# Optimization experiments

Hardware: AMD Instinct MI355X
Metric: run time of the kernel (lower is better)

## Reference

```python
import jax, jax.numpy as jnp
import numpy as np

EPS = 1e-5
TAU = 0.1

def _bn(x, g, b):
    # BatchNorm1d in training mode: batch statistics (biased variance)
    mu = jnp.mean(x, axis=0, keepdims=True)
    var = jnp.var(x, axis=0, keepdims=True)
    return (x - mu) * jax.lax.rsqrt(var + EPS) * g + b

def setup_inputs():
    key = jax.random.key(0)
    ks = jax.random.split(key, 8)
    B, D, H, L, P, C, ND, NP = 32768, 2048, 1024, 384, 192, 10, 2, 2
    s = 0.02
    u = jax.random.uniform(ks[7], (B, NP), minval=1e-6, maxval=1.0 - 1e-6)
    return {
        'x': jax.random.normal(ks[0], (B, D), dtype=jnp.float32),
        'W_pre': jax.random.normal(ks[1], (H, D), dtype=jnp.float32) * s,
        'b_pre': jnp.zeros((H,), jnp.float32),
        'g_pre': jnp.ones((H,), jnp.float32),
        'be_pre': jnp.zeros((H,), jnp.float32),
        'W_disc': jax.random.normal(ks[2], (L, H), dtype=jnp.float32) * s,
        'b_disc': jnp.zeros((L,), jnp.float32),
        'g_disc': jnp.ones((L,), jnp.float32),
        'be_disc': jnp.zeros((L,), jnp.float32),
        'W_dfc': jax.random.normal(ks[3], (ND, L), dtype=jnp.float32) * s,
        'b_dfc': jnp.zeros((ND,), jnp.float32),
        'W_sw': jax.random.normal(ks[4], (NP, L), dtype=jnp.float32) * s,
        'b_sw': jnp.zeros((NP,), jnp.float32),
        'W1': jax.random.normal(ks[5], (NP, P, H), dtype=jnp.float32) * s,
        'b1': jnp.zeros((NP, P), jnp.float32),
        'W2': jax.random.normal(ks[6], (NP, C, P), dtype=jnp.float32) * s,
        'b2': jnp.zeros((NP, C), jnp.float32),
        'gumbel_noise': -jnp.log(-jnp.log(u)),
    }

def reference(x, W_pre, b_pre, g_pre, be_pre, W_disc, b_disc, g_disc, be_disc,
              W_dfc, b_dfc, W_sw, b_sw, W1, b1, W2, b2, gumbel_noise):
    # pre_classifier: Linear + BN + ReLU
    feature = jax.nn.relu(_bn(x @ W_pre.T + b_pre, g_pre, be_pre))
    # GRL is identity in forward
    dp = jax.nn.relu(_bn(feature @ W_disc.T + b_disc, g_disc, be_disc))
    dom = dp @ W_dfc.T + b_dfc                      # [B, num_domains]
    sw = jax.nn.relu(dp @ W_sw.T + b_sw)            # [B, n_partition]
    gum = jax.nn.softmax((sw + gumbel_noise) / TAU, axis=-1)  # soft gumbel-softmax
    idx = jnp.argmax(gum, axis=-1)                  # [B] routing decision
    # compute both (tiny) experts densely, then select per sample (faithful math,
    # avoids per-sample gather of full weight matrices)
    h_all = jax.nn.relu(jnp.einsum('bd,epd->bep', feature, W1) + b1)  # [B,E,P]
    o_all = jnp.einsum('bep,ecp->bec', h_all, W2) + b2                # [B,E,C]
    out = jnp.take_along_axis(o_all, idx[:, None, None], axis=1)[:, 0]  # [B,C]
    # original: sum_p gum[b,p] * stacked (stacked has one entry) == out * sum(gum)
    cop = out * jnp.sum(gum, axis=-1, keepdims=True)
    return cop, dom, idx
```

## Files before the change

kernel.cpp:

```cpp
#include <hip/hip_runtime.h>
#include <math.h>

#define kB 32768
#define kD 2048
#define kH 1024
#define kL 384
#define kP 192
#define kC 10
#define kNP 2
#define kND 2
#define kNCAT 768
#define kTAU 0.1f
#define kEPS 1e-5f
#define NPART 256
#define SCALE 64.0f
#define INV_SC2 (1.0f / 4096.0f)

typedef _Float16 f16x8 __attribute__((ext_vector_type(8)));
typedef _Float16 f16x4 __attribute__((ext_vector_type(4)));
typedef float f32x4 __attribute__((ext_vector_type(4)));

__device__ __forceinline__ void gll16(const unsigned short* g, unsigned short* l)
{
    __builtin_amdgcn_global_load_lds(
        (const __attribute__((address_space(1))) unsigned int*)g,
        (__attribute__((address_space(3))) unsigned int*)l, 16, 0, 0);
}

__global__ __launch_bounds__(256)
void split_pack(const float* __restrict__ in, unsigned short* __restrict__ out, int K)
{
    const int row = blockIdx.x;
    const int t = threadIdx.x;
    const int s = row & 7;
    const float* ir = in + (size_t)row * K;
    unsigned short* orow = out + (size_t)row * (K * 2);
    for (int k0 = t * 4; k0 < K; k0 += 1024) {
        const float4 v = *(const float4*)&ir[k0];
        const float a0 = v.x * SCALE, a1 = v.y * SCALE, a2 = v.z * SCALE, a3 = v.w * SCALE;
        const _Float16 h0 = (_Float16)a0, h1 = (_Float16)a1, h2 = (_Float16)a2, h3 = (_Float16)a3;
        const _Float16 l0 = (_Float16)(a0 - (float)h0), l1 = (_Float16)(a1 - (float)h1);
        const _Float16 l2 = (_Float16)(a2 - (float)h2), l3 = (_Float16)(a3 - (float)h3);
        const f16x4 hi = {h0, h1, h2, h3};
        const f16x4 lo = {l0, l1, l2, l3};
        const int kb = k0 >> 5, kk = k0 & 31;
        const int c = kk >> 3, off = kk & 7;
        *(f16x4*)&orow[kb * 64 + ((c ^ s) << 3) + off]       = hi;
        *(f16x4*)&orow[kb * 64 + (((c ^ 4) ^ s) << 3) + off] = lo;
    }
}

template<int KDIM, bool BN>
__global__ __launch_bounds__(512, 1)
void gemm_fused(const float* __restrict__ Afp,
                const unsigned short* __restrict__ Bpk,
                const float* __restrict__ bnsc, const float* __restrict__ bnsh,
                float* __restrict__ C, const int N, const int gridX,
                float* __restrict__ psum, float* __restrict__ psumsq, const int statN)
{
    constexpr int NKB = KDIM / 32;
    __shared__ unsigned short lds[4][256 * 64];

    const int t = threadIdx.x;
    const int lane = t & 63;
    const int w = t >> 6;
    const int wr = w >> 2, wc = w & 3;
    const int lr = lane & 15, lg = lane >> 4;
    const int ca = (lg ^ (lr & 7)) * 8;

    const int nwg = gridDim.x;
    const int chunk = nwg >> 3;
    const int bid = blockIdx.x;
    const int logical = (bid & 7) * chunk + (bid >> 3);
    const int bx = logical % gridX, by = logical / gridX;
    const int m0 = by * 256, n0 = bx * 256;

    const int arow = t >> 1;
    const int akh = t & 1;
    const int s7 = arow & 7;
    const int c0 = akh * 2, c1 = akh * 2 + 1;
    const float* aSrc = Afp + (size_t)(m0 + arow) * KDIM + akh * 16;

    const size_t bstride = (size_t)NKB * 64;
    const unsigned short* bG[4];
    int bLoff[4];
#pragma unroll
    for (int it = 0; it < 4; ++it) {
        const int Q = (w * 4 + it) * 64 + lane;
        bG[it] = Bpk + (size_t)(n0 + (Q >> 3)) * bstride + (Q & 7) * 8;
        bLoff[it] = (w * 4 + it) * 512;
    }

    f32x4 acc[8][4];
#pragma unroll
    for (int mi = 0; mi < 8; ++mi)
#pragma unroll
        for (int ni = 0; ni < 4; ++ni) acc[mi][ni] = (f32x4){0.f, 0.f, 0.f, 0.f};

    float4 av[4], scv[4], shv[4];

    auto stage_issue = [&](int kb, int buf) {
        const int kt = kb * 32;
#pragma unroll
        for (int it = 0; it < 4; ++it)
            gll16(bG[it] + (size_t)kb * 64, &lds[2 + buf][bLoff[it]]);
#pragma unroll
        for (int j = 0; j < 4; ++j)
            av[j] = *(const float4*)&aSrc[kt + j * 4];
        if constexpr (BN) {
#pragma unroll
            for (int j = 0; j < 4; ++j) {
                scv[j] = *(const float4*)&bnsc[kt + akh * 16 + j * 4];
                shv[j] = *(const float4*)&bnsh[kt + akh * 16 + j * 4];
            }
        }
    };

    auto stage_write = [&](int buf) {
        float v[16];
#pragma unroll
        for (int j = 0; j < 4; ++j) {
            float4 a = av[j];
            if constexpr (BN) {
                a.x = fmaxf(fmaf(a.x, scv[j].x, shv[j].x), 0.f);
                a.y = fmaxf(fmaf(a.y, scv[j].y, shv[j].y), 0.f);
                a.z = fmaxf(fmaf(a.z, scv[j].z, shv[j].z), 0.f);
                a.w = fmaxf(fmaf(a.w, scv[j].w, shv[j].w), 0.f);
            } else {
                a.x *= SCALE; a.y *= SCALE; a.z *= SCALE; a.w *= SCALE;
            }
            v[j * 4 + 0] = a.x; v[j * 4 + 1] = a.y;
            v[j * 4 + 2] = a.z; v[j * 4 + 3] = a.w;
        }
        f16x8 hi[2], lo[2];
#pragma unroll
        for (int h = 0; h < 2; ++h)
#pragma unroll
            for (int i = 0; i < 8; ++i) {
                const float x = v[h * 8 + i];
                const _Float16 hh = (_Float16)x;
                hi[h][i] = hh;
                lo[h][i] = (_Float16)(x - (float)hh);
            }
        unsigned short* dst = &lds[buf][arow * 64];
        *(f16x8*)&dst[(c0 ^ s7) * 8]       = hi[0];
        *(f16x8*)&dst[(c1 ^ s7) * 8]       = hi[1];
        *(f16x8*)&dst[((c0 ^ 4) ^ s7) * 8] = lo[0];
        *(f16x8*)&dst[((c1 ^ 4) ^ s7) * 8] = lo[1];
    };

    stage_issue(0, 0);
    stage_write(0);
    asm volatile("s_waitcnt vmcnt(0) lgkmcnt(0)" ::: "memory");
    __builtin_amdgcn_s_barrier();

    for (int kb = 0; kb < NKB; ++kb) {
        const int cur = kb & 1, nxt = cur ^ 1;
        const bool pf = (kb + 1 < NKB);
        if (pf) stage_issue(kb + 1, nxt);

        f16x8 bh[4], bl[4];
#pragma unroll
        for (int ni = 0; ni < 4; ++ni) {
            const unsigned short* bb = &lds[2 + cur][(wc * 64 + ni * 16 + lr) * 64];
            bh[ni] = *(const f16x8*)&bb[ca];
            bl[ni] = *(const f16x8*)&bb[ca ^ 32];
        }
#pragma unroll
        for (int mi = 0; mi < 8; ++mi) {
            const unsigned short* ab = &lds[cur][(wr * 128 + mi * 16 + lr) * 64];
            const f16x8 ah = *(const f16x8*)&ab[ca];
            const f16x8 al = *(const f16x8*)&ab[ca ^ 32];
#pragma unroll
            for (int ni = 0; ni < 4; ++ni)
                acc[mi][ni] = __builtin_amdgcn_mfma_f32_16x16x32_f16(ah, bh[ni], acc[mi][ni], 0, 0, 0);
#pragma unroll
            for (int ni = 0; ni < 4; ++ni)
                acc[mi][ni] = __builtin_amdgcn_mfma_f32_16x16x32_f16(ah, bl[ni], acc[mi][ni], 0, 0, 0);
#pragma unroll
            for (int ni = 0; ni < 4; ++ni)
                acc[mi][ni] = __builtin_amdgcn_mfma_f32_16x16x32_f16(al, bh[ni], acc[mi][ni], 0, 0, 0);
        }
        if (pf) stage_write(nxt);
        asm volatile("s_waitcnt vmcnt(0) lgkmcnt(0)" ::: "memory");
        __builtin_amdgcn_s_barrier();
    }

#pragma unroll
    for (int mi = 0; mi < 8; ++mi)
#pragma unroll
        for (int j = 0; j < 4; ++j) {
            const int row = m0 + wr * 128 + mi * 16 + lg * 4 + j;
            float* cr = C + (size_t)row * N + n0 + wc * 64 + lr;
#pragma unroll
            for (int ni = 0; ni < 4; ++ni) cr[ni * 16] = acc[mi][ni][j];
        }

#pragma unroll
    for (int ni = 0; ni < 4; ++ni) {
        float s = 0.f, sq = 0.f;
#pragma unroll
        for (int mi = 0; mi < 8; ++mi)
#pragma unroll
            for (int j = 0; j < 4; ++j) {
                const float v = acc[mi][ni][j];
                s += v;
                sq = fmaf(v, v, sq);
            }
        s  += __shfl_xor(s, 16);  s  += __shfl_xor(s, 32);
        sq += __shfl_xor(sq, 16); sq += __shfl_xor(sq, 32);
        const int col = n0 + wc * 64 + ni * 16 + lr;
        if (lane < 16 && col < statN) {
            psum[(size_t)(by * 2 + wr) * statN + col]   = s;
            psumsq[(size_t)(by * 2 + wr) * statN + col] = sq;
        }
    }
}

__global__ __launch_bounds__(256)
void colstat_finalize(const float* __restrict__ psum, const float* __restrict__ psumsq,
                      int ncols, const float* __restrict__ g, const float* __restrict__ be,
                      float* __restrict__ scale, float* __restrict__ shift,
                      float inv_sc, float outsc)
{
    const int c = blockIdx.x * 256 + threadIdx.x;
    if (c >= ncols) return;
    float s = 0.f, sq = 0.f;
    for (int i = 0; i < NPART; ++i) {
        s  += psum[(size_t)i * ncols + c];
        sq += psumsq[(size_t)i * ncols + c];
    }
    const float mup = s * (1.f / kB);
    const float var = (sq * (1.f / kB) - mup * mup) * inv_sc * inv_sc;
    const float scl = outsc * g[c] * rsqrtf(var + kEPS) * inv_sc;
    scale[c] = scl;
    shift[c] = fmaf(-mup, scl, outsc * be[c]);
}

__global__ __launch_bounds__(256)
void tail_kernel(const float* __restrict__ Z2,
                 const float* __restrict__ scale2, const float* __restrict__ shift2,
                 const float* __restrict__ W_dfc, const float* __restrict__ b_dfc,
                 const float* __restrict__ W_sw, const float* __restrict__ b_sw,
                 const float* __restrict__ b1, const float* __restrict__ W2,
                 const float* __restrict__ b2, const float* __restrict__ noise,
                 float* __restrict__ out)
{
    __shared__ float sWdfc[kND * kL];
    __shared__ float sWsw[kNP * kL];
    __shared__ float sW2[kNP * kC * kP];
    __shared__ float sb1[kNP * kP];
    __shared__ float sScale[kL];
    __shared__ float sShift[kL];
    const int t = threadIdx.x;
    for (int i = t; i < kND * kL; i += 256) sWdfc[i] = W_dfc[i];
    for (int i = t; i < kNP * kL; i += 256) sWsw[i] = W_sw[i];
    for (int i = t; i < kNP * kC * kP; i += 256) sW2[i] = W2[i];
    for (int i = t; i < kNP * kP; i += 256) sb1[i] = b1[i];
    for (int i = t; i < kL; i += 256) { sScale[i] = scale2[i]; sShift[i] = shift2[i]; }
    __syncthreads();

    const int lane = t & 63;
    const int b = blockIdx.x * 4 + (t >> 6);
    const float* z = Z2 + (size_t)b * kNCAT;

    float d0 = 0.f, d1 = 0.f, s0 = 0.f, s1 = 0.f;
#pragma unroll
    for (int j = 0; j < 6; ++j) {
        const int k = lane + j * 64;
        const float dp = fmaxf(fmaf(z[k], sScale[k], sShift[k]), 0.f);
        d0 = fmaf(dp, sWdfc[k],      d0);
        d1 = fmaf(dp, sWdfc[kL + k], d1);
        s0 = fmaf(dp, sWsw[k],       s0);
        s1 = fmaf(dp, sWsw[kL + k],  s1);
    }
#pragma unroll
    for (int off = 32; off; off >>= 1) {
        d0 += __shfl_xor(d0, off);
        d1 += __shfl_xor(d1, off);
        s0 += __shfl_xor(s0, off);
        s1 += __shfl_xor(s1, off);
    }
    d0 += b_dfc[0];
    d1 += b_dfc[1];

    const float sw0 = fmaxf(s0 + b_sw[0], 0.f);
    const float sw1 = fmaxf(s1 + b_sw[1], 0.f);
    const float l0 = (sw0 + noise[(size_t)b * 2 + 0]) * (1.f / kTAU);
    const float l1 = (sw1 + noise[(size_t)b * 2 + 1]) * (1.f / kTAU);
    const float mx = fmaxf(l0, l1);
    const float e0 = expf(l0 - mx), e1 = expf(l1 - mx);
    const float inv = 1.f / (e0 + e1);
    const float sgum = e0 * inv + e1 * inv;
    const int idx = (l1 > l0) ? 1 : 0;

    const float* zh = z + kL + idx * kP;
    const float h0 = fmaxf(fmaf(zh[lane],       INV_SC2, sb1[idx * kP + lane]),       0.f);
    const float h1 = fmaxf(fmaf(zh[lane + 64],  INV_SC2, sb1[idx * kP + lane + 64]),  0.f);
    const float h2 = fmaxf(fmaf(zh[lane + 128], INV_SC2, sb1[idx * kP + lane + 128]), 0.f);

    float* cop  = out;
    float* dom  = out + (size_t)kB * kC;
    float* idxo = dom + (size_t)kB * kND;

#pragma unroll
    for (int c = 0; c < kC; ++c) {
        const float* wv = &sW2[(idx * kC + c) * kP];
        float oc = h0 * wv[lane] + h1 * wv[lane + 64] + h2 * wv[lane + 128];
#pragma unroll
        for (int off = 32; off; off >>= 1) oc += __shfl_xor(oc, off);
        if (lane == c) cop[(size_t)b * kC + c] = (oc + b2[idx * kC + c]) * sgum;
    }
    if (lane == 0) {
        dom[(size_t)b * 2 + 0] = d0;
        dom[(size_t)b * 2 + 1] = d1;
        idxo[b] = (float)idx;
    }
}

extern "C" void kernel_launch(void* const* d_in, const int* in_sizes, int n_in,
                              void* d_out, int out_size, void* d_ws, size_t ws_size,
                              hipStream_t stream)
{
    const float* x       = (const float*)d_in[0];
    const float* W_pre   = (const float*)d_in[1];
    const float* g_pre   = (const float*)d_in[3];
    const float* be_pre  = (const float*)d_in[4];
    const float* W_disc  = (const float*)d_in[5];
    const float* g_disc  = (const float*)d_in[7];
    const float* be_disc = (const float*)d_in[8];
    const float* W_dfc   = (const float*)d_in[9];
    const float* b_dfc   = (const float*)d_in[10];
    const float* W_sw    = (const float*)d_in[11];
    const float* b_sw    = (const float*)d_in[12];
    const float* W1      = (const float*)d_in[13];
    const float* b1      = (const float*)d_in[14];
    const float* W2      = (const float*)d_in[15];
    const float* b2      = (const float*)d_in[16];
    const float* noise   = (const float*)d_in[17];

    char* wsb = (char*)d_ws;
    unsigned short* Wps = (unsigned short*)wsb;
    unsigned short* Ws2 = (unsigned short*)(wsb + (size_t)1024 * 4096 * 2);
    float* Z1 = (float*)(wsb + (size_t)1024 * 4096 * 2 + (size_t)768 * 2048 * 2);
    float* Z2 = Z1 + (size_t)kB * kH;
    float* psum1  = Z2 + (size_t)kB * kNCAT;
    float* psq1   = psum1 + (size_t)NPART * kH;
    float* psum2  = psq1 + (size_t)NPART * kH;
    float* psq2   = psum2 + (size_t)NPART * kL;
    float* scale1 = psq2 + (size_t)NPART * kL;
    float* shift1 = scale1 + kH;
    float* scale2 = shift1 + kH;
    float* shift2 = scale2 + kL;
    float* out    = (float*)d_out;

    split_pack<<<dim3(kH), 256, 0, stream>>>(W_pre, Wps, kD);
    split_pack<<<dim3(kL), 256, 0, stream>>>(W_disc, Ws2, kH);
    split_pack<<<dim3(kNP * kP), 256, 0, stream>>>(W1, Ws2 + (size_t)kL * (2 * kH), kH);
    gemm_fused<kD, false><<<dim3(4 * 128), 512, 0, stream>>>(
        x, Wps, nullptr, nullptr, Z1, kH, 4, psum1, psq1, kH);
    colstat_finalize<<<dim3(kH / 256), 256, 0, stream>>>(psum1, psq1, kH, g_pre, be_pre,
                                                         scale1, shift1, INV_SC2, SCALE);
    gemm_fused<kH, true><<<dim3(3 * 128), 512, 0, stream>>>(
        Z1, Ws2, scale1, shift1, Z2, kNCAT, 3, psum2, psq2, kL);
    colstat_finalize<<<dim3((kL + 255) / 256), 256, 0, stream>>>(psum2, psq2, kL, g_disc, be_disc,
                                                                 scale2, shift2, INV_SC2, 1.0f);
    tail_kernel<<<dim3(kB / 4), 256, 0, stream>>>(Z2, scale2, shift2, W_dfc, b_dfc,
                                                  W_sw, b_sw, b1, W2, b2, noise, out);
}
```

Before: 650.5 us.

## Switch GEMM inner loop to 32x32x16 MFMA with new LDS swizzle key

```diff
diff --git a/kernel.cpp b/kernel.cpp
--- a/kernel.cpp
+++ b/kernel.cpp
@@ -18,7 +18,7 @@
 
 typedef _Float16 f16x8 __attribute__((ext_vector_type(8)));
 typedef _Float16 f16x4 __attribute__((ext_vector_type(4)));
-typedef float f32x4 __attribute__((ext_vector_type(4)));
+typedef float f32x16 __attribute__((ext_vector_type(16)));
 
 __device__ __forceinline__ void gll16(const unsigned short* g, unsigned short* l)
 {
@@ -27,12 +27,14 @@
         (__attribute__((address_space(3))) unsigned int*)l, 16, 0, 0);
 }
 
+__device__ __host__ __forceinline__ int key8(int r) { return (r ^ (r >> 3)) & 7; }
+
 __global__ __launch_bounds__(256)
 void split_pack(const float* __restrict__ in, unsigned short* __restrict__ out, int K)
 {
     const int row = blockIdx.x;
     const int t = threadIdx.x;
-    const int s = row & 7;
+    const int s = key8(row);
     const float* ir = in + (size_t)row * K;
     unsigned short* orow = out + (size_t)row * (K * 2);
     for (int k0 = t * 4; k0 < K; k0 += 1024) {
@@ -65,8 +67,7 @@
     const int lane = t & 63;
     const int w = t >> 6;
     const int wr = w >> 2, wc = w & 3;
-    const int lr = lane & 15, lg = lane >> 4;
-    const int ca = (lg ^ (lr & 7)) * 8;
+    const int l31 = lane & 31, kg = lane >> 5;
 
     const int nwg = gridDim.x;
     const int chunk = nwg >> 3;
@@ -77,7 +78,7 @@
 
     const int arow = t >> 1;
     const int akh = t & 1;
-    const int s7 = arow & 7;
+    const int skey = key8(arow);
     const int c0 = akh * 2, c1 = akh * 2 + 1;
     const float* aSrc = Afp + (size_t)(m0 + arow) * KDIM + akh * 16;
 
@@ -91,11 +92,21 @@
         bLoff[it] = (w * 4 + it) * 512;
     }
 
-    f32x4 acc[8][4];
-#pragma unroll
-    for (int mi = 0; mi < 8; ++mi)
-#pragma unroll
-        for (int ni = 0; ni < 4; ++ni) acc[mi][ni] = (f32x4){0.f, 0.f, 0.f, 0.f};
+    int keyA[4], keyB[2];
+#pragma unroll
+    for (int mi = 0; mi < 4; ++mi)
+        keyA[mi] = (l31 & 7) ^ ((mi * 4 + (l31 >> 3)) & 7);
+#pragma unroll
+    for (int ni = 0; ni < 2; ++ni)
+        keyB[ni] = (l31 & 7) ^ ((wc * 8 + ni * 4 + (l31 >> 3)) & 7);
+
+    f32x16 acc[4][2];
+#pragma unroll
+    for (int mi = 0; mi < 4; ++mi)
+#pragma unroll
+        for (int ni = 0; ni < 2; ++ni)
+#pragma unroll
+            for (int r = 0; r < 16; ++r) acc[mi][ni][r] = 0.f;
 
     float4 av[4], scv[4], shv[4];
 
@@ -143,10 +154,10 @@
                 lo[h][i] = (_Float16)(x - (float)hh);
             }
         unsigned short* dst = &lds[buf][arow * 64];
-        *(f16x8*)&dst[(c0 ^ s7) * 8]       = hi[0];
-        *(f16x8*)&dst[(c1 ^ s7) * 8]       = hi[1];
-        *(f16x8*)&dst[((c0 ^ 4) ^ s7) * 8] = lo[0];
-        *(f16x8*)&dst[((c1 ^ 4) ^ s7) * 8] = lo[1];
+        *(f16x8*)&dst[(c0 ^ skey) * 8]       = hi[0];
+        *(f16x8*)&dst[(c1 ^ skey) * 8]       = hi[1];
+        *(f16x8*)&dst[((c0 ^ 4) ^ skey) * 8] = lo[0];
+        *(f16x8*)&dst[((c1 ^ 4) ^ skey) * 8] = lo[1];
     };
 
     stage_issue(0, 0);
@@ -159,27 +170,35 @@
         const bool pf = (kb + 1 < NKB);
         if (pf) stage_issue(kb + 1, nxt);
 
-        f16x8 bh[4], bl[4];
-#pragma unroll
-        for (int ni = 0; ni < 4; ++ni) {
-            const unsigned short* bb = &lds[2 + cur][(wc * 64 + ni * 16 + lr) * 64];
-            bh[ni] = *(const f16x8*)&bb[ca];
-            bl[ni] = *(const f16x8*)&bb[ca ^ 32];
-        }
-#pragma unroll
-        for (int mi = 0; mi < 8; ++mi) {
-            const unsigned short* ab = &lds[cur][(wr * 128 + mi * 16 + lr) * 64];
-            const f16x8 ah = *(const f16x8*)&ab[ca];
-            const f16x8 al = *(const f16x8*)&ab[ca ^ 32];
-#pragma unroll
-            for (int ni = 0; ni < 4; ++ni)
-                acc[mi][ni] = __builtin_amdgcn_mfma_f32_16x16x32_f16(ah, bh[ni], acc[mi][ni], 0, 0, 0);
-#pragma unroll
-            for (int ni = 0; ni < 4; ++ni)
-                acc[mi][ni] = __builtin_amdgcn_mfma_f32_16x16x32_f16(ah, bl[ni], acc[mi][ni], 0, 0, 0);
-#pragma unroll
-            for (int ni = 0; ni < 4; ++ni)
-                acc[mi][ni] = __builtin_amdgcn_mfma_f32_16x16x32_f16(al, bh[ni], acc[mi][ni], 0, 0, 0);
+        f16x8 bh[2][2], bl[2][2];
+#pragma unroll
+        for (int ni = 0; ni < 2; ++ni) {
+            const unsigned short* bb = &lds[2 + cur][(wc * 64 + ni * 32 + l31) * 64];
+#pragma unroll
+            for (int ks = 0; ks < 2; ++ks) {
+                const int lg = ks * 2 + kg;
+                bh[ni][ks] = *(const f16x8*)&bb[((lg ^ keyB[ni]) << 3)];
+                bl[ni][ks] = *(const f16x8*)&bb[(((lg ^ 4) ^ keyB[ni]) << 3)];
+            }
+        }
+#pragma unroll
+        for (int mi = 0; mi < 4; ++mi) {
+            const unsigned short* ab = &lds[cur][(wr * 128 + mi * 32 + l31) * 64];
+            f16x8 ah[2], al[2];
+#pragma unroll
+            for (int ks = 0; ks < 2; ++ks) {
+                const int lg = ks * 2 + kg;
+                ah[ks] = *(const f16x8*)&ab[((lg ^ keyA[mi]) << 3)];
+                al[ks] = *(const f16x8*)&ab[(((lg ^ 4) ^ keyA[mi]) << 3)];
+            }
+#pragma unroll
+            for (int ni = 0; ni < 2; ++ni)
+#pragma unroll
+                for (int ks = 0; ks < 2; ++ks) {
+                    acc[mi][ni] = __builtin_amdgcn_mfma_f32_32x32x16_f16(ah[ks], bh[ni][ks], acc[mi][ni], 0, 0, 0);
+                    acc[mi][ni] = __builtin_amdgcn_mfma_f32_32x32x16_f16(ah[ks], bl[ni][ks], acc[mi][ni], 0, 0, 0);
+                    acc[mi][ni] = __builtin_amdgcn_mfma_f32_32x32x16_f16(al[ks], bh[ni][ks], acc[mi][ni], 0, 0, 0);
+                }
         }
         if (pf) stage_write(nxt);
         asm volatile("s_waitcnt vmcnt(0) lgkmcnt(0)" ::: "memory");
@@ -187,30 +206,32 @@
     }
 
 #pragma unroll
-    for (int mi = 0; mi < 8; ++mi)
-#pragma unroll
-        for (int j = 0; j < 4; ++j) {
-            const int row = m0 + wr * 128 + mi * 16 + lg * 4 + j;
-            float* cr = C + (size_t)row * N + n0 + wc * 64 + lr;
-#pragma unroll
-            for (int ni = 0; ni < 4; ++ni) cr[ni * 16] = acc[mi][ni][j];
-        }
-
-#pragma unroll
-    for (int ni = 0; ni < 4; ++ni) {
+    for (int mi = 0; mi < 4; ++mi)
+#pragma unroll
+        for (int ni = 0; ni < 2; ++ni) {
+            const int colg = n0 + wc * 64 + ni * 32 + l31;
+#pragma unroll
+            for (int r = 0; r < 16; ++r) {
+                const int row = m0 + wr * 128 + mi * 32 + (r & 3) + 8 * (r >> 2) + 4 * kg;
+                C[(size_t)row * N + colg] = acc[mi][ni][r];
+            }
+        }
+
+#pragma unroll
+    for (int ni = 0; ni < 2; ++ni) {
         float s = 0.f, sq = 0.f;
 #pragma unroll
-        for (int mi = 0; mi < 8; ++mi)
-#pragma unroll
-            for (int j = 0; j < 4; ++j) {
-                const float v = acc[mi][ni][j];
+        for (int mi = 0; mi < 4; ++mi)
+#pragma unroll
+            for (int r = 0; r < 16; ++r) {
+                const float v = acc[mi][ni][r];
                 s += v;
                 sq = fmaf(v, v, sq);
             }
-        s  += __shfl_xor(s, 16);  s  += __shfl_xor(s, 32);
-        sq += __shfl_xor(sq, 16); sq += __shfl_xor(sq, 32);
-        const int col = n0 + wc * 64 + ni * 16 + lr;
-        if (lane < 16 && col < statN) {
+        s  += __shfl_xor(s, 32);
+        sq += __shfl_xor(sq, 32);
+        const int col = n0 + wc * 64 + ni * 32 + l31;
+        if (lane < 32 && col < statN) {
             psum[(size_t)(by * 2 + wr) * statN + col]   = s;
             psumsq[(size_t)(by * 2 + wr) * statN + col] = sq;
         }
```

After: 691.1 us. +6.2%, slower.

## Deepen GEMM pipeline with two-stage A prefetch, LDS BN params, new swizzle, narrower tile

Applied to the files above, without the earlier changes.

```diff
diff --git a/kernel.cpp b/kernel.cpp
--- a/kernel.cpp
+++ b/kernel.cpp
@@ -20,6 +20,10 @@
 typedef _Float16 f16x4 __attribute__((ext_vector_type(4)));
 typedef float f32x4 __attribute__((ext_vector_type(4)));
 
+#define WAITVM4   asm volatile("s_waitcnt vmcnt(4)" ::: "memory")
+#define WAITVM0   asm volatile("s_waitcnt vmcnt(0)" ::: "memory")
+#define WAITLGKM0 asm volatile("s_waitcnt lgkmcnt(0)" ::: "memory")
+
 __device__ __forceinline__ void gll16(const unsigned short* g, unsigned short* l)
 {
     __builtin_amdgcn_global_load_lds(
@@ -27,12 +31,17 @@
         (__attribute__((address_space(3))) unsigned int*)l, 16, 0, 0);
 }
 
+__device__ __host__ __forceinline__ int wkey(int r)
+{
+    return (r & 1) | ((r & 2) << 1) | ((r & 4) >> 1);
+}
+
 __global__ __launch_bounds__(256)
 void split_pack(const float* __restrict__ in, unsigned short* __restrict__ out, int K)
 {
     const int row = blockIdx.x;
     const int t = threadIdx.x;
-    const int s = row & 7;
+    const int s = wkey(row & 7);
     const float* ir = in + (size_t)row * K;
     unsigned short* orow = out + (size_t)row * (K * 2);
     for (int k0 = t * 4; k0 < K; k0 += 1024) {
@@ -50,7 +59,7 @@
     }
 }
 
-template<int KDIM, bool BN>
+template<int KDIM, int TILEN, bool BN>
 __global__ __launch_bounds__(512, 1)
 void gemm_fused(const float* __restrict__ Afp,
                 const unsigned short* __restrict__ Bpk,
@@ -59,73 +68,77 @@
                 float* __restrict__ psum, float* __restrict__ psumsq, const int statN)
 {
     constexpr int NKB = KDIM / 32;
-    __shared__ unsigned short lds[4][256 * 64];
+    constexpr int NI = TILEN / 64;
+    constexpr int BG = TILEN / 64;
+    __shared__ __align__(16) unsigned short As_[2][256 * 64];
+    __shared__ __align__(16) unsigned short Bs_[2][TILEN * 64];
+    __shared__ float sScL[BN ? KDIM : 1];
+    __shared__ float sShL[BN ? KDIM : 1];
 
     const int t = threadIdx.x;
     const int lane = t & 63;
     const int w = t >> 6;
     const int wr = w >> 2, wc = w & 3;
     const int lr = lane & 15, lg = lane >> 4;
-    const int ca = (lg ^ (lr & 7)) * 8;
+    const int ca = (lg ^ wkey(lane & 7)) * 8;
 
     const int nwg = gridDim.x;
     const int chunk = nwg >> 3;
     const int bid = blockIdx.x;
     const int logical = (bid & 7) * chunk + (bid >> 3);
     const int bx = logical % gridX, by = logical / gridX;
-    const int m0 = by * 256, n0 = bx * 256;
+    const int m0 = by * 256, n0 = bx * TILEN;
 
     const int arow = t >> 1;
     const int akh = t & 1;
-    const int s7 = arow & 7;
+    const int skey = wkey(arow & 7);
     const int c0 = akh * 2, c1 = akh * 2 + 1;
     const float* aSrc = Afp + (size_t)(m0 + arow) * KDIM + akh * 16;
 
     const size_t bstride = (size_t)NKB * 64;
-    const unsigned short* bG[4];
-    int bLoff[4];
-#pragma unroll
-    for (int it = 0; it < 4; ++it) {
-        const int Q = (w * 4 + it) * 64 + lane;
+    const unsigned short* bG[BG];
+    int bLoff[BG];
+#pragma unroll
+    for (int it = 0; it < BG; ++it) {
+        const int Q = (w * BG + it) * 64 + lane;
         bG[it] = Bpk + (size_t)(n0 + (Q >> 3)) * bstride + (Q & 7) * 8;
-        bLoff[it] = (w * 4 + it) * 512;
-    }
-
-    f32x4 acc[8][4];
+        bLoff[it] = (w * BG + it) * 512;
+    }
+
+    f32x4 acc[8][NI];
 #pragma unroll
     for (int mi = 0; mi < 8; ++mi)
 #pragma unroll
-        for (int ni = 0; ni < 4; ++ni) acc[mi][ni] = (f32x4){0.f, 0.f, 0.f, 0.f};
-
-    float4 av[4], scv[4], shv[4];
-
-    auto stage_issue = [&](int kb, int buf) {
+        for (int ni = 0; ni < NI; ++ni) acc[mi][ni] = (f32x4){0.f, 0.f, 0.f, 0.f};
+
+    float4 av0[4], av1[4];
+
+    auto issueA = [&](float4 (&av)[4], int kb) {
         const int kt = kb * 32;
-#pragma unroll
-        for (int it = 0; it < 4; ++it)
-            gll16(bG[it] + (size_t)kb * 64, &lds[2 + buf][bLoff[it]]);
 #pragma unroll
         for (int j = 0; j < 4; ++j)
             av[j] = *(const float4*)&aSrc[kt + j * 4];
-        if constexpr (BN) {
-#pragma unroll
-            for (int j = 0; j < 4; ++j) {
-                scv[j] = *(const float4*)&bnsc[kt + akh * 16 + j * 4];
-                shv[j] = *(const float4*)&bnsh[kt + akh * 16 + j * 4];
-            }
-        }
     };
 
-    auto stage_write = [&](int buf) {
+    auto gllB = [&](int kb, int buf) {
+#pragma unroll
+        for (int it = 0; it < BG; ++it)
+            gll16(bG[it] + (size_t)kb * 64, &Bs_[buf][bLoff[it]]);
+    };
+
+    auto writeA = [&](const float4 (&av)[4], int buf, int tile) {
+        const int kt = tile * 32 + akh * 16;
         float v[16];
 #pragma unroll
         for (int j = 0; j < 4; ++j) {
             float4 a = av[j];
             if constexpr (BN) {
-                a.x = fmaxf(fmaf(a.x, scv[j].x, shv[j].x), 0.f);
-                a.y = fmaxf(fmaf(a.y, scv[j].y, shv[j].y), 0.f);
-                a.z = fmaxf(fmaf(a.z, scv[j].z, shv[j].z), 0.f);
-                a.w = fmaxf(fmaf(a.w, scv[j].w, shv[j].w), 0.f);
+                const float4 sc = *(const float4*)&sScL[kt + j * 4];
+                const float4 sh = *(const float4*)&sShL[kt + j * 4];
+                a.x = fmaxf(fmaf(a.x, sc.x, sh.x), 0.f);
+                a.y = fmaxf(fmaf(a.y, sc.y, sh.y), 0.f);
+                a.z = fmaxf(fmaf(a.z, sc.z, sh.z), 0.f);
+                a.w = fmaxf(fmaf(a.w, sc.w, sh.w), 0.f);
             } else {
                 a.x *= SCALE; a.y *= SCALE; a.z *= SCALE; a.w *= SCALE;
             }
@@ -142,48 +155,74 @@
                 hi[h][i] = hh;
                 lo[h][i] = (_Float16)(x - (float)hh);
             }
-        unsigned short* dst = &lds[buf][arow * 64];
-        *(f16x8*)&dst[(c0 ^ s7) * 8]       = hi[0];
-        *(f16x8*)&dst[(c1 ^ s7) * 8]       = hi[1];
-        *(f16x8*)&dst[((c0 ^ 4) ^ s7) * 8] = lo[0];
-        *(f16x8*)&dst[((c1 ^ 4) ^ s7) * 8] = lo[1];
+        unsigned short* dst = &As_[buf][arow * 64];
+        *(f16x8*)&dst[(c0 ^ skey) * 8]       = hi[0];
+        *(f16x8*)&dst[(c1 ^ skey) * 8]       = hi[1];
+        *(f16x8*)&dst[((c0 ^ 4) ^ skey) * 8] = lo[0];
+        *(f16x8*)&dst[((c1 ^ 4) ^ skey) * 8] = lo[1];
     };
 
-    stage_issue(0, 0);
-    stage_write(0);
-    asm volatile("s_waitcnt vmcnt(0) lgkmcnt(0)" ::: "memory");
-    __builtin_amdgcn_s_barrier();
-
-    for (int kb = 0; kb < NKB; ++kb) {
+    auto body = [&](int kb, const float4 (&avW)[4], float4 (&avI)[4]) {
         const int cur = kb & 1, nxt = cur ^ 1;
-        const bool pf = (kb + 1 < NKB);
-        if (pf) stage_issue(kb + 1, nxt);
-
-        f16x8 bh[4], bl[4];
-#pragma unroll
-        for (int ni = 0; ni < 4; ++ni) {
-            const unsigned short* bb = &lds[2 + cur][(wc * 64 + ni * 16 + lr) * 64];
+        if (kb + 1 < NKB) {
+            writeA(avW, nxt, kb + 1);
+            gllB(kb + 1, nxt);
+        }
+        __builtin_amdgcn_sched_barrier(0);
+        if (kb + 2 < NKB) issueA(avI, kb + 2);
+
+        f16x8 bh[NI], bl[NI];
+#pragma unroll
+        for (int ni = 0; ni < NI; ++ni) {
+            const unsigned short* bb = &Bs_[cur][(wc * (16 * NI) + ni * 16 + lr) * 64];
             bh[ni] = *(const f16x8*)&bb[ca];
             bl[ni] = *(const f16x8*)&bb[ca ^ 32];
         }
 #pragma unroll
         for (int mi = 0; mi < 8; ++mi) {
-            const unsigned short* ab = &lds[cur][(wr * 128 + mi * 16 + lr) * 64];
+            const unsigned short* ab = &As_[cur][(wr * 128 + mi * 16 + lr) * 64];
             const f16x8 ah = *(const f16x8*)&ab[ca];
             const f16x8 al = *(const f16x8*)&ab[ca ^ 32];
 #pragma unroll
-            for (int ni = 0; ni < 4; ++ni)
+            for (int ni = 0; ni < NI; ++ni)
                 acc[mi][ni] = __builtin_amdgcn_mfma_f32_16x16x32_f16(ah, bh[ni], acc[mi][ni], 0, 0, 0);
 #pragma unroll
-            for (int ni = 0; ni < 4; ++ni)
+            for (int ni = 0; ni < NI; ++ni)
                 acc[mi][ni] = __builtin_amdgcn_mfma_f32_16x16x32_f16(ah, bl[ni], acc[mi][ni], 0, 0, 0);
 #pragma unroll
-            for (int ni = 0; ni < 4; ++ni)
+            for (int ni = 0; ni < NI; ++ni)
                 acc[mi][ni] = __builtin_amdgcn_mfma_f32_16x16x32_f16(al, bh[ni], acc[mi][ni], 0, 0, 0);
         }
-        if (pf) stage_write(nxt);
-        asm volatile("s_waitcnt vmcnt(0) lgkmcnt(0)" ::: "memory");
-        __builtin_amdgcn_s_barrier();
+        if (kb + 1 < NKB) {
+            if (kb + 2 < NKB) { WAITVM4; } else { WAITVM0; }
+            WAITLGKM0;
+            __builtin_amdgcn_sched_barrier(0);
+            __builtin_amdgcn_s_barrier();
+            __builtin_amdgcn_sched_barrier(0);
+        }
+    };
+
+    if constexpr (BN) {
+        if (t < KDIM / 4) {
+            ((float4*)sScL)[t] = ((const float4*)bnsc)[t];
+            ((float4*)sShL)[t] = ((const float4*)bnsh)[t];
+        }
+        __syncthreads();
+    }
+    issueA(av0, 0);
+    gllB(0, 0);
+    __builtin_amdgcn_sched_barrier(0);
+    issueA(av1, 1);
+    writeA(av0, 0, 0);
+    WAITVM4;
+    WAITLGKM0;
+    __builtin_amdgcn_sched_barrier(0);
+    __builtin_amdgcn_s_barrier();
+    __builtin_amdgcn_sched_barrier(0);
+
+    for (int kb = 0; kb < NKB; kb += 2) {
+        body(kb,     av1, av0);
+        body(kb + 1, av0, av1);
     }
 
 #pragma unroll
@@ -191,13 +230,13 @@
 #pragma unroll
         for (int j = 0; j < 4; ++j) {
             const int row = m0 + wr * 128 + mi * 16 + lg * 4 + j;
-            float* cr = C + (size_t)row * N + n0 + wc * 64 + lr;
-#pragma unroll
-            for (int ni = 0; ni < 4; ++ni) cr[ni * 16] = acc[mi][ni][j];
-        }
-
-#pragma unroll
-    for (int ni = 0; ni < 4; ++ni) {
+            float* cr = C + (size_t)row * N + n0 + wc * (16 * NI) + lr;
+#pragma unroll
+            for (int ni = 0; ni < NI; ++ni) cr[ni * 16] = acc[mi][ni][j];
+        }
+
+#pragma unroll
+    for (int ni = 0; ni < NI; ++ni) {
         float s = 0.f, sq = 0.f;
 #pragma unroll
         for (int mi = 0; mi < 8; ++mi)
@@ -209,7 +248,7 @@
             }
         s  += __shfl_xor(s, 16);  s  += __shfl_xor(s, 32);
         sq += __shfl_xor(sq, 16); sq += __shfl_xor(sq, 32);
-        const int col = n0 + wc * 64 + ni * 16 + lr;
+        const int col = n0 + wc * (16 * NI) + ni * 16 + lr;
         if (lane < 16 && col < statN) {
             psum[(size_t)(by * 2 + wr) * statN + col]   = s;
             psumsq[(size_t)(by * 2 + wr) * statN + col] = sq;
@@ -357,12 +396,12 @@
     split_pack<<<dim3(kH), 256, 0, stream>>>(W_pre, Wps, kD);
     split_pack<<<dim3(kL), 256, 0, stream>>>(W_disc, Ws2, kH);
     split_pack<<<dim3(kNP * kP), 256, 0, stream>>>(W1, Ws2 + (size_t)kL * (2 * kH), kH);
-    gemm_fused<kD, false><<<dim3(4 * 128), 512, 0, stream>>>(
+    gemm_fused<kD, 256, false><<<dim3(4 * 128), 512, 0, stream>>>(
         x, Wps, nullptr, nullptr, Z1, kH, 4, psum1, psq1, kH);
     colstat_finalize<<<dim3(kH / 256), 256, 0, stream>>>(psum1, psq1, kH, g_pre, be_pre,
                                                          scale1, shift1, INV_SC2, SCALE);
-    gemm_fused<kH, true><<<dim3(3 * 128), 512, 0, stream>>>(
-        Z1, Ws2, scale1, shift1, Z2, kNCAT, 3, psum2, psq2, kL);
+    gemm_fused<kH, 128, true><<<dim3(6 * 128), 512, 0, stream>>>(
+        Z1, Ws2, scale1, shift1, Z2, kNCAT, 6, psum2, psq2, kL);
     colstat_finalize<<<dim3((kL + 255) / 256), 256, 0, stream>>>(psum2, psq2, kL, g_disc, be_disc,
                                                                  scale2, shift2, INV_SC2, 1.0f);
     tail_kernel<<<dim3(kB / 4), 256, 0, stream>>>(Z2, scale2, shift2, W_dfc, b_dfc,
```

Result: slower. 671.7 us (+3.3%).

## Shrink GEMM tiles to 128x128 with 256 threads, multiple blocks per CU

Applied to the files above, without the earlier changes.

```diff
diff --git a/kernel.cpp b/kernel.cpp
--- a/kernel.cpp
+++ b/kernel.cpp
@@ -12,7 +12,7 @@
 #define kNCAT 768
 #define kTAU 0.1f
 #define kEPS 1e-5f
-#define NPART 256
+#define NPART 512
 #define SCALE 64.0f
 #define INV_SC2 (1.0f / 4096.0f)
 
@@ -20,6 +20,12 @@
 typedef _Float16 f16x4 __attribute__((ext_vector_type(4)));
 typedef float f32x4 __attribute__((ext_vector_type(4)));
 
+#define WAITVM0   asm volatile("s_waitcnt vmcnt(0)" ::: "memory")
+#define WAITVM4   asm volatile("s_waitcnt vmcnt(4)" ::: "memory")
+#define WAITLGKM0 asm volatile("s_waitcnt lgkmcnt(0)" ::: "memory")
+#define SB0       __builtin_amdgcn_sched_barrier(0)
+#define BAR       __builtin_amdgcn_s_barrier()
+
 __device__ __forceinline__ void gll16(const unsigned short* g, unsigned short* l)
 {
     __builtin_amdgcn_global_load_lds(
@@ -27,12 +33,17 @@
         (__attribute__((address_space(3))) unsigned int*)l, 16, 0, 0);
 }
 
+__device__ __host__ __forceinline__ int wkey(int r)
+{
+    return (r & 1) | ((r & 2) << 1) | ((r & 4) >> 1);
+}
+
 __global__ __launch_bounds__(256)
 void split_pack(const float* __restrict__ in, unsigned short* __restrict__ out, int K)
 {
     const int row = blockIdx.x;
     const int t = threadIdx.x;
-    const int s = row & 7;
+    const int s = wkey(row & 7);
     const float* ir = in + (size_t)row * K;
     unsigned short* orow = out + (size_t)row * (K * 2);
     for (int k0 = t * 4; k0 < K; k0 += 1024) {
@@ -51,7 +62,7 @@
 }
 
 template<int KDIM, bool BN>
-__global__ __launch_bounds__(512, 1)
+__global__ __launch_bounds__(256, 3)
 void gemm_fused(const float* __restrict__ Afp,
                 const unsigned short* __restrict__ Bpk,
                 const float* __restrict__ bnsc, const float* __restrict__ bnsh,
@@ -59,25 +70,28 @@
                 float* __restrict__ psum, float* __restrict__ psumsq, const int statN)
 {
     constexpr int NKB = KDIM / 32;
-    __shared__ unsigned short lds[4][256 * 64];
+    __shared__ __align__(16) unsigned short As_[128 * 64];
+    __shared__ __align__(16) unsigned short Bs_[128 * 64];
+    __shared__ float sScL[BN ? KDIM : 4];
+    __shared__ float sShL[BN ? KDIM : 4];
 
     const int t = threadIdx.x;
     const int lane = t & 63;
     const int w = t >> 6;
-    const int wr = w >> 2, wc = w & 3;
+    const int wr = w >> 1, wc = w & 1;
     const int lr = lane & 15, lg = lane >> 4;
-    const int ca = (lg ^ (lr & 7)) * 8;
+    const int ca = (lg ^ wkey(lane & 7)) * 8;
 
     const int nwg = gridDim.x;
     const int chunk = nwg >> 3;
     const int bid = blockIdx.x;
     const int logical = (bid & 7) * chunk + (bid >> 3);
     const int bx = logical % gridX, by = logical / gridX;
-    const int m0 = by * 256, n0 = bx * 256;
+    const int m0 = by * 128, n0 = bx * 128;
 
     const int arow = t >> 1;
     const int akh = t & 1;
-    const int s7 = arow & 7;
+    const int skey = wkey(arow & 7);
     const int c0 = akh * 2, c1 = akh * 2 + 1;
     const float* aSrc = Afp + (size_t)(m0 + arow) * KDIM + akh * 16;
 
@@ -91,41 +105,40 @@
         bLoff[it] = (w * 4 + it) * 512;
     }
 
-    f32x4 acc[8][4];
-#pragma unroll
-    for (int mi = 0; mi < 8; ++mi)
+    f32x4 acc[4][4];
+#pragma unroll
+    for (int mi = 0; mi < 4; ++mi)
 #pragma unroll
         for (int ni = 0; ni < 4; ++ni) acc[mi][ni] = (f32x4){0.f, 0.f, 0.f, 0.f};
 
-    float4 av[4], scv[4], shv[4];
-
-    auto stage_issue = [&](int kb, int buf) {
+    float4 av[4];
+
+    auto issueA = [&](int kb) {
         const int kt = kb * 32;
-#pragma unroll
-        for (int it = 0; it < 4; ++it)
-            gll16(bG[it] + (size_t)kb * 64, &lds[2 + buf][bLoff[it]]);
 #pragma unroll
         for (int j = 0; j < 4; ++j)
             av[j] = *(const float4*)&aSrc[kt + j * 4];
-        if constexpr (BN) {
-#pragma unroll
-            for (int j = 0; j < 4; ++j) {
-                scv[j] = *(const float4*)&bnsc[kt + akh * 16 + j * 4];
-                shv[j] = *(const float4*)&bnsh[kt + akh * 16 + j * 4];
-            }
-        }
     };
 
-    auto stage_write = [&](int buf) {
+    auto gllB = [&](int kb) {
+#pragma unroll
+        for (int it = 0; it < 4; ++it)
+            gll16(bG[it] + (size_t)kb * 64, &Bs_[bLoff[it]]);
+    };
+
+    auto writeA = [&](int tile) {
+        const int kt = tile * 32 + akh * 16;
         float v[16];
 #pragma unroll
         for (int j = 0; j < 4; ++j) {
             float4 a = av[j];
             if constexpr (BN) {
-                a.x = fmaxf(fmaf(a.x, scv[j].x, shv[j].x), 0.f);
-                a.y = fmaxf(fmaf(a.y, scv[j].y, shv[j].y), 0.f);
-                a.z = fmaxf(fmaf(a.z, scv[j].z, shv[j].z), 0.f);
-                a.w = fmaxf(fmaf(a.w, scv[j].w, shv[j].w), 0.f);
+                const float4 sc = *(const float4*)&sScL[kt + j * 4];
+                const float4 sh = *(const float4*)&sShL[kt + j * 4];
+                a.x = fmaxf(fmaf(a.x, sc.x, sh.x), 0.f);
+                a.y = fmaxf(fmaf(a.y, sc.y, sh.y), 0.f);
+                a.z = fmaxf(fmaf(a.z, sc.z, sh.z), 0.f);
+                a.w = fmaxf(fmaf(a.w, sc.w, sh.w), 0.f);
             } else {
                 a.x *= SCALE; a.y *= SCALE; a.z *= SCALE; a.w *= SCALE;
             }
@@ -142,33 +155,47 @@
                 hi[h][i] = hh;
                 lo[h][i] = (_Float16)(x - (float)hh);
             }
-        unsigned short* dst = &lds[buf][arow * 64];
-        *(f16x8*)&dst[(c0 ^ s7) * 8]       = hi[0];
-        *(f16x8*)&dst[(c1 ^ s7) * 8]       = hi[1];
-        *(f16x8*)&dst[((c0 ^ 4) ^ s7) * 8] = lo[0];
-        *(f16x8*)&dst[((c1 ^ 4) ^ s7) * 8] = lo[1];
+        unsigned short* dst = &As_[arow * 64];
+        *(f16x8*)&dst[(c0 ^ skey) * 8]       = hi[0];
+        *(f16x8*)&dst[(c1 ^ skey) * 8]       = hi[1];
+        *(f16x8*)&dst[((c0 ^ 4) ^ skey) * 8] = lo[0];
+        *(f16x8*)&dst[((c1 ^ 4) ^ skey) * 8] = lo[1];
     };
 
-    stage_issue(0, 0);
-    stage_write(0);
-    asm volatile("s_waitcnt vmcnt(0) lgkmcnt(0)" ::: "memory");
-    __builtin_amdgcn_s_barrier();
-
-    for (int kb = 0; kb < NKB; ++kb) {
-        const int cur = kb & 1, nxt = cur ^ 1;
-        const bool pf = (kb + 1 < NKB);
-        if (pf) stage_issue(kb + 1, nxt);
+    if constexpr (BN) {
+        for (int i = t; i < KDIM / 4; i += 256) {
+            ((float4*)sScL)[i] = ((const float4*)bnsc)[i];
+            ((float4*)sShL)[i] = ((const float4*)bnsh)[i];
+        }
+        __syncthreads();
+    }
+    issueA(0);
+
+    for (int s = 0; s < NKB; ++s) {
+        const bool pf = (s + 1 < NKB);
+        BAR;
+        WAITVM0;
+        SB0;
+        writeA(s);
+        gllB(s);
+        SB0;
+        if (pf) issueA(s + 1);
+        SB0;
+        if (pf) { WAITVM4; } else { WAITVM0; }
+        WAITLGKM0;
+        SB0;
+        BAR;
 
         f16x8 bh[4], bl[4];
 #pragma unroll
         for (int ni = 0; ni < 4; ++ni) {
-            const unsigned short* bb = &lds[2 + cur][(wc * 64 + ni * 16 + lr) * 64];
+            const unsigned short* bb = &Bs_[(wc * 64 + ni * 16 + lr) * 64];
             bh[ni] = *(const f16x8*)&bb[ca];
             bl[ni] = *(const f16x8*)&bb[ca ^ 32];
         }
 #pragma unroll
-        for (int mi = 0; mi < 8; ++mi) {
-            const unsigned short* ab = &lds[cur][(wr * 128 + mi * 16 + lr) * 64];
+        for (int mi = 0; mi < 4; ++mi) {
+            const unsigned short* ab = &As_[(wr * 64 + mi * 16 + lr) * 64];
             const f16x8 ah = *(const f16x8*)&ab[ca];
             const f16x8 al = *(const f16x8*)&ab[ca ^ 32];
 #pragma unroll
@@ -181,16 +208,13 @@
             for (int ni = 0; ni < 4; ++ni)
                 acc[mi][ni] = __builtin_amdgcn_mfma_f32_16x16x32_f16(al, bh[ni], acc[mi][ni], 0, 0, 0);
         }
-        if (pf) stage_write(nxt);
-        asm volatile("s_waitcnt vmcnt(0) lgkmcnt(0)" ::: "memory");
-        __builtin_amdgcn_s_barrier();
-    }
-
-#pragma unroll
-    for (int mi = 0; mi < 8; ++mi)
+    }
+
+#pragma unroll
+    for (int mi = 0; mi < 4; ++mi)
 #pragma unroll
         for (int j = 0; j < 4; ++j) {
-            const int row = m0 + wr * 128 + mi * 16 + lg * 4 + j;
+            const int row = m0 + wr * 64 + mi * 16 + lg * 4 + j;
             float* cr = C + (size_t)row * N + n0 + wc * 64 + lr;
 #pragma unroll
             for (int ni = 0; ni < 4; ++ni) cr[ni * 16] = acc[mi][ni][j];
@@ -200,7 +224,7 @@
     for (int ni = 0; ni < 4; ++ni) {
         float s = 0.f, sq = 0.f;
 #pragma unroll
-        for (int mi = 0; mi < 8; ++mi)
+        for (int mi = 0; mi < 4; ++mi)
 #pragma unroll
             for (int j = 0; j < 4; ++j) {
                 const float v = acc[mi][ni][j];
@@ -357,12 +381,12 @@
     split_pack<<<dim3(kH), 256, 0, stream>>>(W_pre, Wps, kD);
     split_pack<<<dim3(kL), 256, 0, stream>>>(W_disc, Ws2, kH);
     split_pack<<<dim3(kNP * kP), 256, 0, stream>>>(W1, Ws2 + (size_t)kL * (2 * kH), kH);
-    gemm_fused<kD, false><<<dim3(4 * 128), 512, 0, stream>>>(
-        x, Wps, nullptr, nullptr, Z1, kH, 4, psum1, psq1, kH);
+    gemm_fused<kD, false><<<dim3(8 * 256), 256, 0, stream>>>(
+        x, Wps, nullptr, nullptr, Z1, kH, 8, psum1, psq1, kH);
     colstat_finalize<<<dim3(kH / 256), 256, 0, stream>>>(psum1, psq1, kH, g_pre, be_pre,
                                                          scale1, shift1, INV_SC2, SCALE);
-    gemm_fused<kH, true><<<dim3(3 * 128), 512, 0, stream>>>(
-        Z1, Ws2, scale1, shift1, Z2, kNCAT, 3, psum2, psq2, kL);
+    gemm_fused<kH, true><<<dim3(6 * 256), 256, 0, stream>>>(
+        Z1, Ws2, scale1, shift1, Z2, kNCAT, 6, psum2, psq2, kL);
     colstat_finalize<<<dim3((kL + 255) / 256), 256, 0, stream>>>(psum2, psq2, kL, g_disc, be_disc,
                                                                  scale2, shift2, INV_SC2, 1.0f);
     tail_kernel<<<dim3(kB / 4), 256, 0, stream>>>(Z2, scale2, shift2, W_dfc, b_dfc,
```

After: 724.8 us. 11.4% more time.
